# Performance work log

Hardware: AMD Instinct MI355X
Metric: run time of the kernel (lower is better)

## Reference

```python
import jax, jax.numpy as jnp
import numpy as np

TIME_WINDOW = 500  # matches init_kwargs time_window


def setup_inputs() -> dict:
    key = jax.random.key(0)
    # 512x512 image flattened to a vector of Poisson rates in [0, 1)
    img = jax.random.uniform(key, (262144,), dtype=jnp.float32)
    return {"img": img}


def reference(img):
    # Original loop: for each pixel i, draw time_window Poisson counts t_j ~ Poisson(img[i]);
    # for each j with t_j > 0, set encoded[i, j : j + t_j] = 1 (clipped to the window).
    # Position k is set iff there exists j <= k with j + t_j > k, i.e. cummax_j(j + t_j) > k.
    N = img.shape[0]
    T = TIME_WINDOW
    key = jax.random.key(42)
    counts = jax.random.poisson(key, img[:, None], shape=(N, T))  # [N, T] int
    cols = jnp.arange(T, dtype=counts.dtype)[None, :]             # [1, T]
    ends = counts + cols                                          # j + t_j
    run_max = jax.lax.cummax(ends, axis=1)                        # max_{j<=k} (j + t_j)
    spikes = run_max > cols                                       # [N, T] bool
    return spikes.T                                               # [T, N] as in original
```

## Files before the change

### kernel.cpp

```cpp
#include <hip/hip_runtime.h>
#include <stdint.h>


#define TWIN 500
#define HALF 250
#define WARM 26
#define NKEYS 32
#define DCAP 30
#define BLOCK 1024
#define XPITCH 9

struct Subkeys {
  uint32_t a[NKEYS];
  uint32_t b[NKEYS];
};

__host__ __device__ __forceinline__ uint32_t rotl32(uint32_t x, uint32_t r) {
#if defined(__HIP_DEVICE_COMPILE__) && __has_builtin(__builtin_amdgcn_alignbit)
  return __builtin_amdgcn_alignbit(x, x, 32u - r);
#else
  return (x << r) | (x >> (32u - r));
#endif
}

__host__ __device__ __forceinline__ void tf2x32(uint32_t k0, uint32_t k1,
                                                uint32_t x0, uint32_t x1,
                                                uint32_t& o0, uint32_t& o1) {
  const uint32_t ks2 = k0 ^ k1 ^ 0x1BD11BDAu;
  x0 += k0; x1 += k1;
#define TF_RND(r) { x0 += x1; x1 = rotl32(x1, (r)); x1 ^= x0; }
  TF_RND(13) TF_RND(15) TF_RND(26) TF_RND(6)
  x0 += k1;  x1 += ks2 + 1u;
  TF_RND(17) TF_RND(29) TF_RND(16) TF_RND(24)
  x0 += ks2; x1 += k0 + 2u;
  TF_RND(13) TF_RND(15) TF_RND(26) TF_RND(6)
  x0 += k0;  x1 += k1 + 3u;
  TF_RND(17) TF_RND(29) TF_RND(16) TF_RND(24)
  x0 += k1;  x1 += ks2 + 4u;
  TF_RND(13) TF_RND(15) TF_RND(26) TF_RND(6)
  x0 += ks2; x1 += k0 + 5u;
#undef TF_RND
  o0 = x0; o1 = x1;
}

__device__ __forceinline__ float cephes_logf(float u) {
  float x = fmaxf(u, __uint_as_float(0x00800000u));
  int emm0 = (int)(__float_as_uint(x) >> 23);
  x = __uint_as_float((__float_as_uint(x) & 0x807FFFFFu) | 0x3F000000u);
  float e = (float)(emm0 - 127) + 1.0f;
  const bool mask = x < 0.707106781186547524f;
  float tmp = mask ? x : 0.0f;
  x = x - 1.0f;
  e = e - (mask ? 1.0f : 0.0f);
  x = x + tmp;
  float z = x * x;
  float y = 7.0376836292E-2f;
  y = fmaf(y, x, -1.1514610310E-1f);
  y = fmaf(y, x,  1.1676998740E-1f);
  y = fmaf(y, x, -1.2420140846E-1f);
  y = fmaf(y, x,  1.4249322787E-1f);
  y = fmaf(y, x, -1.6668057665E-1f);
  y = fmaf(y, x,  2.0000714765E-1f);
  y = fmaf(y, x, -2.4999993993E-1f);
  y = fmaf(y, x,  3.3333331174E-1f);
  y = y * x;
  y = y * z;
  y = fmaf(e, -2.12194440e-4f, y);
  y = fmaf(z, -0.5f, y);
  x = x + y;
  x = fmaf(e, 0.693359375f, x);
  return x;
}

__global__ __attribute__((amdgpu_flat_work_group_size(BLOCK, BLOCK)))
void CustomPoisson_12292196401945_kernel(
    const float* __restrict__ img, int* __restrict__ out,
    Subkeys sk, int N) {
  __shared__ uint2 lk[NKEYS];
  __shared__ unsigned long long sbuf[BLOCK];
  __shared__ uint32_t xbuf[BLOCK * XPITCH];

  const int tid = threadIdx.x;
  if (tid < NKEYS) lk[tid] = make_uint2(sk.a[tid], sk.b[tid]);

  const int hb = N / BLOCK;
  const int b = blockIdx.x;
  const int h = (b >= hb) ? 1 : 0;
  const int pixBase = (b - h * hb) * BLOCK;

  {
    const float lam0 = img[pixBase + tid];
    sbuf[tid] = ((unsigned long long)__float_as_uint(lam0) << 32) | (uint32_t)tid;
  }
  __syncthreads();
  for (int ks = 2; ks <= BLOCK; ks <<= 1) {
    for (int js = ks >> 1; js > 0; js >>= 1) {
      const int p = tid ^ js;
      if (p > tid) {
        const bool up = ((tid & ks) == 0);
        const unsigned long long a = sbuf[tid], c = sbuf[p];
        const bool sw = up ? (a > c) : (a < c);
        if (sw) { sbuf[tid] = c; sbuf[p] = a; }
      }
      __syncthreads();
    }
  }
  const unsigned long long rec = sbuf[tid];
  const uint32_t orig = (uint32_t)rec;
  const float neg_lam = -__uint_as_float((uint32_t)(rec >> 32));

  const uint32_t k0a = sk.a[0], k0b = sk.b[0];
  const int jstart = h ? HALF : 0;
  const uint32_t e_base =
      (uint32_t)(pixBase + (int)orig) * TWIN + (uint32_t)jstart;

  int jj = h ? -WARM : 0;
  float S = 0.0f;
  int k = 0, d = 0;
  uint32_t cka = k0a, ckb = k0b;
  int runmax = 0;
  uint32_t cur = 0;

  while (__any(jj < HALF)) {
    if (jj < HALF) {
      const uint2 nk = lk[(uint32_t)(d + 1)];
      const uint32_t ks2 = cka ^ ckb ^ 0x1BD11BDAu;
      uint32_t t0 = cka;
      uint32_t t1 = e_base + (uint32_t)jj + ckb;
      t0 += t1; t1 = rotl32(t1, 13); t1 ^= t0;
      t0 += t1; t1 = rotl32(t1, 15); t1 ^= t0;
      t0 += t1; t1 = rotl32(t1, 26); t1 ^= t0;
      t0 += t1; t1 = rotl32(t1,  6); t1 ^= t0;
      t0 += ckb; t1 += ks2 + 1u;
      t0 += t1; t1 = rotl32(t1, 17); t1 ^= t0;
      t0 += t1; t1 = rotl32(t1, 29); t1 ^= t0;
      t0 += t1; t1 = rotl32(t1, 16); t1 ^= t0;
      t0 += t1; t1 = rotl32(t1, 24); t1 ^= t0;
      t0 += ks2; t1 += cka + 2u;
      t0 += t1; t1 = rotl32(t1, 13); t1 ^= t0;
      t0 += t1; t1 = rotl32(t1, 15); t1 ^= t0;
      t0 += t1; t1 = rotl32(t1, 26); t1 ^= t0;
      t0 += t1; t1 = rotl32(t1,  6); t1 ^= t0;
      t0 += cka; t1 += ckb + 3u;
      t0 += t1; t1 = rotl32(t1, 17); t1 ^= t0;
      t0 += t1; t1 = rotl32(t1, 29); t1 ^= t0;
      t0 += t1; t1 = rotl32(t1, 16); t1 ^= t0;
      t0 += t1; t1 = rotl32(t1, 24); t1 ^= t0;
      t0 += ckb; t1 += ks2 + 4u;
      t0 += t1; t1 = rotl32(t1, 13); t1 ^= t0;
      t0 += t1; t1 = rotl32(t1, 15); t1 ^= t0;
      t0 += t1; t1 = rotl32(t1, 26); t1 ^= t0;
      t0 += t1; t1 = rotl32(t1,  6); t1 ^= t0;
      t0 += ks2; t1 += cka + 5u;
      const uint32_t rb = t0 ^ t1;
      const float u = __uint_as_float((rb >> 9) | 0x3F800000u) - 1.0f;
      S += cephes_logf(u);
      const bool alive = S > neg_lam;
      const int k2 = k + (alive ? 1 : 0);
      const bool fin = (!alive) || (d >= DCAP);
      const int ends = k2 + jstart + jj;
      runmax = runmax > ends ? runmax : ends;
      const bool recb = fin && (jj >= 0);
      const uint32_t bit =
          (uint32_t)((runmax > jstart + jj) ? 1u : 0u) << ((uint32_t)jj & 31u);
      cur |= recb ? bit : 0u;
      const bool flush = recb && (((jj & 31) == 31) || (jj == HALF - 1));
      if (flush) xbuf[orig * XPITCH + (uint32_t)(jj >> 5)] = cur;
      cur = flush ? 0u : cur;
      S = fin ? 0.0f : S;
      k = fin ? 0 : k2;
      d = fin ? 0 : d + 1;
      cka = fin ? k0a : nk.x;
      ckb = fin ? k0b : nk.y;
      jj += fin ? 1 : 0;
    }
  }
  __syncthreads();

  uint32_t off = (uint32_t)jstart * (uint32_t)N + (uint32_t)(pixBase + tid);
  for (int w = 0; w < 8; ++w) {
    const uint32_t word = xbuf[tid * XPITCH + w];
    const int nb = (w < 7) ? 32 : (HALF - 7 * 32);
    #pragma unroll 1
    for (int t2 = 0; t2 < nb; ++t2) {
      out[off] = (int)((word >> t2) & 1u);
      off += (uint32_t)N;
    }
  }
}

extern "C" void kernel_launch(void* const* d_in, const int* in_sizes, int n_in,
                              void* d_out, int out_size, void* d_ws, size_t ws_size,
                              hipStream_t stream) {
  const float* img = (const float*)d_in[0];
  int* out = (int*)d_out;
  const int N = in_sizes[0];

  Subkeys sk;
  uint32_t r0 = 0u, r1 = 42u;
  for (int d = 0; d < NKEYS; ++d) {
    uint32_t s0, s1, n0, n1;
    tf2x32(r0, r1, 0u, 1u, s0, s1);
    tf2x32(r0, r1, 0u, 0u, n0, n1);
    sk.a[d] = s0; sk.b[d] = s1;
    r0 = n0; r1 = n1;
  }

  dim3 block(BLOCK);
  dim3 grid(2 * (N / BLOCK));
  hipLaunchKernelGGL(CustomPoisson_12292196401945_kernel, grid, block, 0, stream,
                     img, out, sk, N);
}
```

Baseline: 740.4 us.

## Split warmup phase, unroll draw loop by two, drop DCAP cap and flush logic

Moves the draw body into a macro and splits the per-pixel loop into a warmup pass over negative indices (only for the second half, with no recording) and a main pass that records bits. Each loop is unrolled twice so the wave-wide any() check runs once per two draws. The running max is rewritten around a per-slot end counter, and the LDS word is written on every finished draw instead of only at flush points. Dropping the DCAP cap removes a per-draw check but changes behaviour when more than thirty draws survive, and the unconditional LDS writes add store traffic.

```diff
diff --git a/kernel.cpp b/kernel.cpp
--- a/kernel.cpp
+++ b/kernel.cpp
@@ -6,7 +6,6 @@
 #define HALF 250
 #define WARM 26
 #define NKEYS 32
-#define DCAP 30
 #define BLOCK 1024
 #define XPITCH 9
 
@@ -72,6 +71,57 @@
   return x;
 }
 
+#define DRAW(DO_REC)                                                        \
+  {                                                                         \
+    const uint2 nk = lk[(uint32_t)(d + 1)];                                 \
+    const uint32_t ks2 = cka ^ ckb ^ 0x1BD11BDAu;                           \
+    uint32_t t0 = cka;                                     \
+    uint32_t t1 = e_base + (uint32_t)jj + ckb;             \
+    t0 += t1; t1 = rotl32(t1, 13); t1 ^= t0;                                \
+    t0 += t1; t1 = rotl32(t1, 15); t1 ^= t0;                                \
+    t0 += t1; t1 = rotl32(t1, 26); t1 ^= t0;                                \
+    t0 += t1; t1 = rotl32(t1,  6); t1 ^= t0;                                \
+    t0 += ckb; t1 += ks2 + 1u;                                              \
+    t0 += t1; t1 = rotl32(t1, 17); t1 ^= t0;                                \
+    t0 += t1; t1 = rotl32(t1, 29); t1 ^= t0;                                \
+    t0 += t1; t1 = rotl32(t1, 16); t1 ^= t0;                                \
+    t0 += t1; t1 = rotl32(t1, 24); t1 ^= t0;                                \
+    t0 += ks2; t1 += cka + 2u;                                              \
+    t0 += t1; t1 = rotl32(t1, 13); t1 ^= t0;                                \
+    t0 += t1; t1 = rotl32(t1, 15); t1 ^= t0;                                \
+    t0 += t1; t1 = rotl32(t1, 26); t1 ^= t0;                                \
+    t0 += t1; t1 = rotl32(t1,  6); t1 ^= t0;                                \
+    t0 += cka; t1 += ckb + 3u;                                              \
+    t0 += t1; t1 = rotl32(t1, 17); t1 ^= t0;                                \
+    t0 += t1; t1 = rotl32(t1, 29); t1 ^= t0;                                \
+    t0 += t1; t1 = rotl32(t1, 16); t1 ^= t0;                                \
+    t0 += t1; t1 = rotl32(t1, 24); t1 ^= t0;                                \
+    t0 += ckb; t1 += ks2 + 4u;                                              \
+    t0 += t1; t1 = rotl32(t1, 13); t1 ^= t0;                                \
+    t0 += t1; t1 = rotl32(t1, 15); t1 ^= t0;                                \
+    t0 += t1; t1 = rotl32(t1, 26); t1 ^= t0;                                \
+    t0 += t1; t1 = rotl32(t1,  6); t1 ^= t0;                                \
+    t0 += ks2; t1 += cka + 5u;                                              \
+    const uint32_t rb = t0 ^ t1;                                            \
+    const float u = __uint_as_float((rb >> 9) | 0x3F800000u) - 1.0f;        \
+    S += cephes_logf(u);                                                    \
+    const bool alive = S > neg_lam;                                         \
+    const int tnx = jj + 1;                                                 \
+    const int ce_eff = ce + (alive ? 1 : 0);              \
+    runm = runm > ce_eff ? runm : ce_eff;         \
+    if (DO_REC) {                                                           \
+      cur |= (runm > jj) ? (1u << ((uint32_t)jj & 31u)) : 0u;               \
+      xbuf[xw_base + ((uint32_t)jj >> 5)] = cur;    \
+    }                                                                       \
+    S   = alive ? S : 0.0f;                                                 \
+    d   = alive ? d + 1 : 0;                                                \
+    cka = alive ? nk.x : k0a;                                               \
+    ckb = alive ? nk.y : k0b;                                               \
+    ce  = alive ? ce_eff : tnx;                                             \
+    jj  = alive ? jj : tnx;                                                 \
+    if (DO_REC) cur = (!alive && ((tnx & 31) == 0)) ? 0u : cur;             \
+  }
+
 __global__ __attribute__((amdgpu_flat_work_group_size(BLOCK, BLOCK)))
 void CustomPoisson_12292196401945_kernel(
     const float* __restrict__ img, int* __restrict__ out,
@@ -113,67 +163,26 @@
   const int jstart = h ? HALF : 0;
   const uint32_t e_base =
       (uint32_t)(pixBase + (int)orig) * TWIN + (uint32_t)jstart;
+  const uint32_t xw_base = orig * XPITCH;
 
   int jj = h ? -WARM : 0;
   float S = 0.0f;
-  int k = 0, d = 0;
+  int d = 0;
   uint32_t cka = k0a, ckb = k0b;
-  int runmax = 0;
+  int ce = jj;
+  int runm = -1000;
   uint32_t cur = 0;
 
+  if (h) {
+    while (__any(jj < 0)) {
+      if (jj < 0) DRAW(false)
+      if (jj < 0) DRAW(false)
+    }
+  }
+
   while (__any(jj < HALF)) {
-    if (jj < HALF) {
-      const uint2 nk = lk[(uint32_t)(d + 1)];
-      const uint32_t ks2 = cka ^ ckb ^ 0x1BD11BDAu;
-      uint32_t t0 = cka;
-      uint32_t t1 = e_base + (uint32_t)jj + ckb;
-      t0 += t1; t1 = rotl32(t1, 13); t1 ^= t0;
-      t0 += t1; t1 = rotl32(t1, 15); t1 ^= t0;
-      t0 += t1; t1 = rotl32(t1, 26); t1 ^= t0;
-      t0 += t1; t1 = rotl32(t1,  6); t1 ^= t0;
-      t0 += ckb; t1 += ks2 + 1u;
-      t0 += t1; t1 = rotl32(t1, 17); t1 ^= t0;
-      t0 += t1; t1 = rotl32(t1, 29); t1 ^= t0;
-      t0 += t1; t1 = rotl32(t1, 16); t1 ^= t0;
-      t0 += t1; t1 = rotl32(t1, 24); t1 ^= t0;
-      t0 += ks2; t1 += cka + 2u;
-      t0 += t1; t1 = rotl32(t1, 13); t1 ^= t0;
-      t0 += t1; t1 = rotl32(t1, 15); t1 ^= t0;
-      t0 += t1; t1 = rotl32(t1, 26); t1 ^= t0;
-      t0 += t1; t1 = rotl32(t1,  6); t1 ^= t0;
-      t0 += cka; t1 += ckb + 3u;
-      t0 += t1; t1 = rotl32(t1, 17); t1 ^= t0;
-      t0 += t1; t1 = rotl32(t1, 29); t1 ^= t0;
-      t0 += t1; t1 = rotl32(t1, 16); t1 ^= t0;
-      t0 += t1; t1 = rotl32(t1, 24); t1 ^= t0;
-      t0 += ckb; t1 += ks2 + 4u;
-      t0 += t1; t1 = rotl32(t1, 13); t1 ^= t0;
-      t0 += t1; t1 = rotl32(t1, 15); t1 ^= t0;
-      t0 += t1; t1 = rotl32(t1, 26); t1 ^= t0;
-      t0 += t1; t1 = rotl32(t1,  6); t1 ^= t0;
-      t0 += ks2; t1 += cka + 5u;
-      const uint32_t rb = t0 ^ t1;
-      const float u = __uint_as_float((rb >> 9) | 0x3F800000u) - 1.0f;
-      S += cephes_logf(u);
-      const bool alive = S > neg_lam;
-      const int k2 = k + (alive ? 1 : 0);
-      const bool fin = (!alive) || (d >= DCAP);
-      const int ends = k2 + jstart + jj;
-      runmax = runmax > ends ? runmax : ends;
-      const bool recb = fin && (jj >= 0);
-      const uint32_t bit =
-          (uint32_t)((runmax > jstart + jj) ? 1u : 0u) << ((uint32_t)jj & 31u);
-      cur |= recb ? bit : 0u;
-      const bool flush = recb && (((jj & 31) == 31) || (jj == HALF - 1));
-      if (flush) xbuf[orig * XPITCH + (uint32_t)(jj >> 5)] = cur;
-      cur = flush ? 0u : cur;
-      S = fin ? 0.0f : S;
-      k = fin ? 0 : k2;
-      d = fin ? 0 : d + 1;
-      cka = fin ? k0a : nk.x;
-      ckb = fin ? k0b : nk.y;
-      jj += fin ? 1 : 0;
-    }
+    if (jj < HALF) DRAW(true)
+    if (jj < HALF) DRAW(true)
   }
   __syncthreads();
 
```

Result: faster. 702.6 us (-5.1%).
